# Performance work log

Measured on AMD Instinct MI355X. Metric: run time of the kernel, lower is better.

The kernel has to match this reference:

```python
import jax, jax.numpy as jnp
import numpy as np
from jax import lax

B, S, D = 4, 4096, 1024
EPS = 1e-6  # flax RMSNorm default epsilon


def setup_inputs() -> dict:
    key = jax.random.key(0)
    ks = jax.random.split(key, 8)
    std = 0.01  # flax.linen.initializers.normal() default stddev
    return {
        "x": jax.random.normal(ks[0], (B, S, D), dtype=jnp.float32),
        "wq": jax.random.normal(ks[1], (D, D), dtype=jnp.float32) * std,
        "wk": jax.random.normal(ks[2], (D, D), dtype=jnp.float32) * std,
        "wv": jax.random.normal(ks[3], (D, D), dtype=jnp.float32) * std,
        "wa": jax.random.normal(ks[4], (D, 2 * D), dtype=jnp.float32) * std,
        "wg": jax.random.normal(ks[5], (D, D), dtype=jnp.float32) * std,
        "wo": jax.random.normal(ks[6], (D, D), dtype=jnp.float32) * std,
        "rms_scale": jnp.ones((D,), dtype=jnp.float32),  # RMSNorm scale param
    }


def gate_loop_operator(k, v, q, a):
    # data-dependent complex linear recurrence: h_t = a_t * h_{t-1} + k_t * v_t
    def binary_operator(e_i, e_j):
        a_i, kv_i = e_i
        a_j, kv_j = e_j
        return (a_j * a_i, a_j * kv_i + kv_j)

    kv = (k * v).astype(jnp.complex64)
    _, y = lax.associative_scan(binary_operator, (a, kv), axis=1)
    return q * jnp.real(y)


def reference(x, wq, wk, wv, wa, wg, wo, rms_scale):
    # RMSNorm (flax default: no mean subtraction, learned scale)
    xn = x * lax.rsqrt(jnp.mean(x * x, axis=-1, keepdims=True) + EPS) * rms_scale

    q = xn @ wq
    k = xn @ wk
    v = xn @ wv
    a = xn @ wa  # [B, S, 2D]
    g = xn @ wg

    a_r, a_i = jnp.split(a, 2, axis=-1)
    a_c = lax.complex(a_r, a_i)
    magnitude = jax.nn.sigmoid(jnp.abs(a_c))  # constrain |a| < 1 for stability
    phase = jnp.angle(a_c)
    a_c = magnitude * jnp.exp(1j * phase)

    y = gate_loop_operator(k, v, q, a_c)
    y = y * jax.nn.silu(g)
    return y @ wo
```

## Files before the change

### kernel.cpp

```cpp
#include <hip/hip_runtime.h>
#include <hip/hip_bf16.h>
#include <math.h>

#define BDIM 4
#define SDIM 4096
#define DDIM 1024
#define MROWS (BDIM*SDIM)
#define EPS 1e-6f
#define NCHUNK 64
#define LCHUNK 64

typedef _Float16 f16_t;
typedef _Float16 f16x4_t __attribute__((ext_vector_type(4)));
typedef _Float16 f16x8_t __attribute__((ext_vector_type(8)));
typedef float    f32x4_t __attribute__((ext_vector_type(4)));

__device__ __forceinline__ void gload16(const void* g, void* l) {
    __builtin_amdgcn_global_load_lds(
        (const __attribute__((address_space(1))) unsigned int*)g,
        (__attribute__((address_space(3))) unsigned int*)l, 16, 0, 0);
}

__global__ __launch_bounds__(256) void fill_kernel(float* __restrict__ out,
                                                   int n, float val)
{
    const int i = blockIdx.x * 256 + threadIdx.x;
    if (i < n) out[i] = val;
}

__global__ __launch_bounds__(256) void rmsnorm_kernel(
    const float* __restrict__ x, const float* __restrict__ scale,
    f16_t* __restrict__ xn)
{
    const int row = blockIdx.x;
    const int tid = threadIdx.x;
    const float4 v = reinterpret_cast<const float4*>(x + (size_t)row * DDIM)[tid];
    float ss = v.x*v.x + v.y*v.y + v.z*v.z + v.w*v.w;
    #pragma unroll
    for (int off = 32; off > 0; off >>= 1)
        ss += __shfl_down(ss, off, 64);
    __shared__ float red[4];
    if ((tid & 63) == 0) red[tid >> 6] = ss;
    __syncthreads();
    ss = red[0] + red[1] + red[2] + red[3];
    const float inv = rsqrtf(ss * (1.0f / DDIM) + EPS);
    const float4 sc = reinterpret_cast<const float4*>(scale)[tid];
    f16x4_t o;
    o.x = (f16_t)(v.x * inv * sc.x);
    o.y = (f16_t)(v.y * inv * sc.y);
    o.z = (f16_t)(v.z * inv * sc.z);
    o.w = (f16_t)(v.w * inv * sc.w);
    reinterpret_cast<f16x4_t*>(xn + (size_t)row * DDIM)[tid] = o;
}

__global__ __launch_bounds__(256) void transpose_f16_kernel(
    const float* __restrict__ W, f16_t* __restrict__ WT, int K, int N)
{
    __shared__ float t[32][33];
    const int kb = blockIdx.y * 32;
    const int nb = blockIdx.x * 32;
    const int r  = threadIdx.x >> 3;
    const int c0 = (threadIdx.x & 7) << 2;
    const float4 v = *reinterpret_cast<const float4*>(&W[(size_t)(kb + r) * N + nb + c0]);
    t[r][c0 + 0] = v.x; t[r][c0 + 1] = v.y; t[r][c0 + 2] = v.z; t[r][c0 + 3] = v.w;
    __syncthreads();
    f16x4_t o;
    o.x = (f16_t)t[c0 + 0][r];
    o.y = (f16_t)t[c0 + 1][r];
    o.z = (f16_t)t[c0 + 2][r];
    o.w = (f16_t)t[c0 + 3][r];
    *reinterpret_cast<f16x4_t*>(&WT[(size_t)(nb + r) * K + kb + c0]) = o;
}

template <int MODE>
__global__ __launch_bounds__(256, 2) void mfma_gemm_kernel(
    const f16_t* __restrict__ A, const f16_t* __restrict__ BT,
    void* __restrict__ Cv, int M, int N, int K)
{
    __shared__ __align__(16) f16_t As[128 * 32];
    __shared__ __align__(16) f16_t Bs[128 * 32];

    const int tid  = threadIdx.x;
    const int wave = tid >> 6;
    const int lane = tid & 63;
    const int bm = blockIdx.y * 128;
    const int bn = blockIdx.x * 128;
    const int wm = (wave & 1) * 64;
    const int wn = (wave >> 1) * 64;

    const int sr = tid >> 2;
    const int sc = (tid & 3) * 8;
    const f16_t* Ag = A  + (size_t)(bm + sr) * K + sc;
    const f16_t* Bg = BT + (size_t)(bn + sr) * K + sc;
    f16_t* Al0 = As + tid * 8;
    f16_t* Al1 = As + 64 * 32 + tid * 8;
    f16_t* Bl0 = Bs + tid * 8;
    f16_t* Bl1 = Bs + 64 * 32 + tid * 8;
    const size_t rowskip = (size_t)64 * K;

    f32x4_t acc[4][4] = {};

    const int fm = lane & 15;
    const int kh = (lane >> 4) << 3;

    for (int kt = 0; kt < K; kt += 32) {
        gload16(Ag + kt, Al0);
        gload16(Ag + rowskip + kt, Al1);
        gload16(Bg + kt, Bl0);
        gload16(Bg + rowskip + kt, Bl1);
        __syncthreads();

        f16x8_t af[4], bfr[4];
        #pragma unroll
        for (int i = 0; i < 4; ++i)
            af[i] = *reinterpret_cast<const f16x8_t*>(&As[(wm + i * 16 + fm) * 32 + kh]);
        #pragma unroll
        for (int j = 0; j < 4; ++j)
            bfr[j] = *reinterpret_cast<const f16x8_t*>(&Bs[(wn + j * 16 + fm) * 32 + kh]);
        #pragma unroll
        for (int i = 0; i < 4; ++i)
            #pragma unroll
            for (int j = 0; j < 4; ++j)
                acc[i][j] = __builtin_amdgcn_mfma_f32_16x16x32_f16(
                    af[i], bfr[j], acc[i][j], 0, 0, 0);
        __syncthreads();
    }

    const int erow = (lane >> 4) << 2;
    const int ecol = lane & 15;
    #pragma unroll
    for (int i = 0; i < 4; ++i) {
        #pragma unroll
        for (int j = 0; j < 4; ++j) {
            const int row0 = bm + wm + i * 16 + erow;
            const int col  = bn + wn + j * 16 + ecol;
            #pragma unroll
            for (int rg = 0; rg < 4; ++rg) {
                const size_t idx = (size_t)(row0 + rg) * N + col;
                const float val = acc[i][j][rg];
                if (MODE == 0) {
                    ((float*)Cv)[idx] = val;
                } else if (MODE == 1) {
                    ((f16_t*)Cv)[idx] = (f16_t)val;
                } else if (MODE == 2) {
                    f16_t* C = (f16_t*)Cv;
                    C[idx] = (f16_t)((float)C[idx] * val);
                } else {
                    float* C = (float*)Cv;
                    const float s = val / (1.0f + expf(-val));
                    C[idx] = C[idx] * s;
                }
            }
        }
    }
}

__global__ __launch_bounds__(256) void atrans_kernel(float* __restrict__ a)
{
    const int i = blockIdx.x * 256 + threadIdx.x;
    const int m = i >> 10;
    const int d = i & 1023;
    const size_t i0 = (size_t)m * (2 * DDIM) + d;
    const float ar = a[i0];
    const float ai = a[i0 + DDIM];
    const float r = sqrtf(ar * ar + ai * ai);
    const float mag = 1.0f / (1.0f + expf(-r));
    if (r > 0.0f) {
        const float s = mag / r;
        a[i0] = ar * s;
        a[i0 + DDIM] = ai * s;
    } else {
        a[i0] = 0.5f;
        a[i0 + DDIM] = 0.0f;
    }
}

__global__ __launch_bounds__(256) void scan1_kernel(
    const float* __restrict__ a, const f16_t* __restrict__ kvb,
    float4* __restrict__ state)
{
    const int t = blockIdx.x * 256 + threadIdx.x;
    const int d = t & 1023;
    const int c = (t >> 10) & (NCHUNK - 1);
    const int b = t >> 16;
    size_t base  = ((size_t)(b * SDIM + c * LCHUNK)) * DDIM + d;
    size_t abase = ((size_t)(b * SDIM + c * LCHUNK)) * (2 * DDIM) + d;
    float Ar = 1.0f, Ai = 0.0f, Hr = 0.0f, Hi = 0.0f;
    for (int s = 0; s < LCHUNK; ++s) {
        const float arr = a[abase];
        const float aii = a[abase + DDIM];
        const float kv = (float)kvb[base];
        const float hr = arr * Hr - aii * Hi + kv;
        const float hi = arr * Hi + aii * Hr;
        Hr = hr; Hi = hi;
        const float nr = arr * Ar - aii * Ai;
        const float ni = arr * Ai + aii * Ar;
        Ar = nr; Ai = ni;
        base += DDIM;
        abase += 2 * DDIM;
    }
    state[t] = make_float4(Ar, Ai, Hr, Hi);
}

__global__ __launch_bounds__(256) void scan2_kernel(
    const float4* __restrict__ state, float2* __restrict__ carry)
{
    const int t = blockIdx.x * 256 + threadIdx.x;
    const int d = t & 1023;
    const int b = t >> 10;
    float cr = 0.0f, ci = 0.0f;
    for (int c = 0; c < NCHUNK; ++c) {
        const size_t idx = ((size_t)(b * NCHUNK + c)) * DDIM + d;
        carry[idx] = make_float2(cr, ci);
        const float4 st = state[idx];
        const float nr = st.x * cr - st.y * ci + st.z;
        const float ni = st.x * ci + st.y * cr + st.w;
        cr = nr; ci = ni;
    }
}

__global__ __launch_bounds__(256) void scan3_kernel(
    const float* __restrict__ a, const f16_t* __restrict__ kvb,
    const float* __restrict__ qg, const float2* __restrict__ carry,
    f16_t* __restrict__ y)
{
    const int t = blockIdx.x * 256 + threadIdx.x;
    const int d = t & 1023;
    const int c = (t >> 10) & (NCHUNK - 1);
    const int b = t >> 16;
    size_t base  = ((size_t)(b * SDIM + c * LCHUNK)) * DDIM + d;
    size_t abase = ((size_t)(b * SDIM + c * LCHUNK)) * (2 * DDIM) + d;
    const float2 h0 = carry[t];
    float Hr = h0.x, Hi = h0.y;
    for (int s = 0; s < LCHUNK; ++s) {
        const float arr = a[abase];
        const float aii = a[abase + DDIM];
        const float kv = (float)kvb[base];
        const float hr = arr * Hr - aii * Hi + kv;
        const float hi = arr * Hi + aii * Hr;
        Hr = hr; Hi = hi;
        y[base] = (f16_t)(qg[base] * Hr);
        base += DDIM;
        abase += 2 * DDIM;
    }
}

extern "C" void kernel_launch(void* const* d_in, const int* in_sizes, int n_in,
                              void* d_out, int out_size, void* d_ws, size_t ws_size,
                              hipStream_t stream)
{
    const float* x        = (const float*)d_in[0];
    const float* wq       = (const float*)d_in[1];
    const float* wk       = (const float*)d_in[2];
    const float* wv       = (const float*)d_in[3];
    const float* wa       = (const float*)d_in[4];
    const float* wg       = (const float*)d_in[5];
    const float* wo       = (const float*)d_in[6];
    const float* rms_scale= (const float*)d_in[7];
    float* out = (float*)d_out;

    const size_t SZ = (size_t)MROWS * DDIM;
    char* ws = (char*)d_ws;
    f16_t* W0   = (f16_t*)ws;
    f16_t* W1   = (f16_t*)(ws + SZ * 2);
    float* W2   = (float*)(ws + SZ * 4);
    f16_t* WT   = (f16_t*)(ws + SZ * 12);
    const size_t WSZ = (size_t)DDIM * DDIM;
    f16_t* WTq = WT;
    f16_t* WTk = WT + WSZ;
    f16_t* WTv = WT + 2 * WSZ;
    f16_t* WTg = WT + 3 * WSZ;
    f16_t* WTo = WT + 4 * WSZ;
    f16_t* WTa = WT + 5 * WSZ;
    float2* carry = (float2*)(ws + SZ * 12 + 7 * WSZ * 2);
    float4* state = (float4*)W0;

    const size_t needed = SZ * 12 + 7 * WSZ * 2
                        + (size_t)BDIM * NCHUNK * DDIM * sizeof(float2);
    if (ws_size < needed) {
        const float marker = (float)(ws_size >> 20);
        fill_kernel<<<(out_size + 255) / 256, 256, 0, stream>>>(out, out_size, marker);
        return;
    }

    rmsnorm_kernel<<<MROWS, 256, 0, stream>>>(x, rms_scale, W0);

    dim3 tblk(256);
    dim3 tg1(DDIM / 32, DDIM / 32);
    dim3 tg2(2 * DDIM / 32, DDIM / 32);
    transpose_f16_kernel<<<tg1, tblk, 0, stream>>>(wq, WTq, DDIM, DDIM);
    transpose_f16_kernel<<<tg1, tblk, 0, stream>>>(wk, WTk, DDIM, DDIM);
    transpose_f16_kernel<<<tg1, tblk, 0, stream>>>(wv, WTv, DDIM, DDIM);
    transpose_f16_kernel<<<tg1, tblk, 0, stream>>>(wg, WTg, DDIM, DDIM);
    transpose_f16_kernel<<<tg1, tblk, 0, stream>>>(wo, WTo, DDIM, DDIM);
    transpose_f16_kernel<<<tg2, tblk, 0, stream>>>(wa, WTa, DDIM, 2 * DDIM);

    dim3 blk(256);
    dim3 g1(DDIM / 128, MROWS / 128);
    dim3 g2(2 * DDIM / 128, MROWS / 128);
    mfma_gemm_kernel<0><<<g1, blk, 0, stream>>>(W0, WTq, out, MROWS, DDIM, DDIM);
    mfma_gemm_kernel<3><<<g1, blk, 0, stream>>>(W0, WTg, out, MROWS, DDIM, DDIM);
    mfma_gemm_kernel<1><<<g1, blk, 0, stream>>>(W0, WTk, W1,  MROWS, DDIM, DDIM);
    mfma_gemm_kernel<2><<<g1, blk, 0, stream>>>(W0, WTv, W1,  MROWS, DDIM, DDIM);
    mfma_gemm_kernel<0><<<g2, blk, 0, stream>>>(W0, WTa, W2,  MROWS, 2 * DDIM, DDIM);

    atrans_kernel<<<(MROWS * DDIM) / 256, 256, 0, stream>>>(W2);

    const int nscan = BDIM * NCHUNK * DDIM;
    scan1_kernel<<<nscan / 256, 256, 0, stream>>>(W2, W1, state);
    scan2_kernel<<<(BDIM * DDIM) / 256, 256, 0, stream>>>(state, carry);
    scan3_kernel<<<nscan / 256, 256, 0, stream>>>(W2, W1, out, carry, W0);

    mfma_gemm_kernel<0><<<g1, blk, 0, stream>>>(W0, WTo, out, MROWS, DDIM, DDIM);
}
```

Before: 654.7 us.

## Fuse Q/K/G projections, interleave complex gate weights, fold gate transform into GEMM

Concatenates the q, k and g projection weights into one N=3072 GEMM that scatters fp16 outputs to separate buffers, replacing three launches. The a-projection weights are column-interleaved so real and imaginary parts land in adjacent columns. The sigmoid-magnitude gate transform then runs in the GEMM epilogue via a lane shuffle, removing the separate atrans pass, and the scans read a as float2. The SiLU gating moves into scan3, and q/g are stored as fp16 in the output buffer, cutting fp32 traffic at the cost of extra q/g rounding and buffer aliasing (carry stored over the weight area).

```diff
diff --git a/kernel.cpp b/kernel.cpp
--- a/kernel.cpp
+++ b/kernel.cpp
@@ -72,10 +72,35 @@
     *reinterpret_cast<f16x4_t*>(&WT[(size_t)(nb + r) * K + kb + c0]) = o;
 }
 
+__global__ __launch_bounds__(256) void transpose_a_kernel(
+    const float* __restrict__ W, f16_t* __restrict__ WT)
+{
+    const int K = DDIM, N = 2 * DDIM;
+    __shared__ float t[32][33];
+    const int kb = blockIdx.y * 32;
+    const int nb = blockIdx.x * 32;
+    const int r  = threadIdx.x >> 3;
+    const int c0 = (threadIdx.x & 7) << 2;
+    const int base = (c0 < 16) ? ((nb >> 1) + c0) : (DDIM + (nb >> 1) + c0 - 16);
+    const float4 v = *reinterpret_cast<const float4*>(&W[(size_t)(kb + r) * N + base]);
+    t[r][c0 + 0] = v.x; t[r][c0 + 1] = v.y; t[r][c0 + 2] = v.z; t[r][c0 + 3] = v.w;
+    __syncthreads();
+    const int rr  = threadIdx.x >> 3;
+    const int cc0 = (threadIdx.x & 7) << 2;
+    const int ctile = (rr >> 1) + (rr & 1) * 16;
+    f16x4_t o;
+    o.x = (f16_t)t[cc0 + 0][ctile];
+    o.y = (f16_t)t[cc0 + 1][ctile];
+    o.z = (f16_t)t[cc0 + 2][ctile];
+    o.w = (f16_t)t[cc0 + 3][ctile];
+    *reinterpret_cast<f16x4_t*>(&WT[(size_t)(nb + rr) * K + kb + cc0]) = o;
+}
+
 template <int MODE>
 __global__ __launch_bounds__(256, 2) void mfma_gemm_kernel(
     const f16_t* __restrict__ A, const f16_t* __restrict__ BT,
-    void* __restrict__ Cv, int M, int N, int K)
+    void* __restrict__ Cv, void* __restrict__ Cv2, void* __restrict__ Cv3,
+    int M, int N, int K)
 {
     __shared__ __align__(16) f16_t As[128 * 32];
     __shared__ __align__(16) f16_t Bs[128 * 32];
@@ -140,38 +165,30 @@
                 const float val = acc[i][j][rg];
                 if (MODE == 0) {
                     ((float*)Cv)[idx] = val;
-                } else if (MODE == 1) {
-                    ((f16_t*)Cv)[idx] = (f16_t)val;
                 } else if (MODE == 2) {
                     f16_t* C = (f16_t*)Cv;
                     C[idx] = (f16_t)((float)C[idx] * val);
+                } else if (MODE == 4) {
+                    const float par = __shfl_xor(val, 1, 64);
+                    const float re = (lane & 1) ? par : val;
+                    const float im = (lane & 1) ? val : par;
+                    const float r = sqrtf(re * re + im * im);
+                    float outv;
+                    if (r > 0.0f) {
+                        const float sg = 1.0f / (1.0f + expf(-r));
+                        outv = val * (sg / r);
+                    } else {
+                        outv = (lane & 1) ? 0.0f : 0.5f;
+                    }
+                    ((float*)Cv)[idx] = outv;
                 } else {
-                    float* C = (float*)Cv;
-                    const float s = val / (1.0f + expf(-val));
-                    C[idx] = C[idx] * s;
+                    f16_t* dst = (bn < 1024) ? (f16_t*)Cv
+                               : (bn < 2048) ? (f16_t*)Cv2 : (f16_t*)Cv3;
+                    const size_t didx = (size_t)(row0 + rg) * DDIM + ((bn & 1023) + wn + j * 16 + ecol);
+                    dst[didx] = (f16_t)val;
                 }
             }
         }
-    }
-}
-
-__global__ __launch_bounds__(256) void atrans_kernel(float* __restrict__ a)
-{
-    const int i = blockIdx.x * 256 + threadIdx.x;
-    const int m = i >> 10;
-    const int d = i & 1023;
-    const size_t i0 = (size_t)m * (2 * DDIM) + d;
-    const float ar = a[i0];
-    const float ai = a[i0 + DDIM];
-    const float r = sqrtf(ar * ar + ai * ai);
-    const float mag = 1.0f / (1.0f + expf(-r));
-    if (r > 0.0f) {
-        const float s = mag / r;
-        a[i0] = ar * s;
-        a[i0 + DDIM] = ai * s;
-    } else {
-        a[i0] = 0.5f;
-        a[i0 + DDIM] = 0.0f;
     }
 }
 
@@ -184,20 +201,18 @@
     const int c = (t >> 10) & (NCHUNK - 1);
     const int b = t >> 16;
     size_t base  = ((size_t)(b * SDIM + c * LCHUNK)) * DDIM + d;
-    size_t abase = ((size_t)(b * SDIM + c * LCHUNK)) * (2 * DDIM) + d;
+    const float2* a2 = (const float2*)a;
     float Ar = 1.0f, Ai = 0.0f, Hr = 0.0f, Hi = 0.0f;
     for (int s = 0; s < LCHUNK; ++s) {
-        const float arr = a[abase];
-        const float aii = a[abase + DDIM];
+        const float2 av = a2[base];
         const float kv = (float)kvb[base];
-        const float hr = arr * Hr - aii * Hi + kv;
-        const float hi = arr * Hi + aii * Hr;
+        const float hr = av.x * Hr - av.y * Hi + kv;
+        const float hi = av.x * Hi + av.y * Hr;
         Hr = hr; Hi = hi;
-        const float nr = arr * Ar - aii * Ai;
-        const float ni = arr * Ai + aii * Ar;
+        const float nr = av.x * Ar - av.y * Ai;
+        const float ni = av.x * Ai + av.y * Ar;
         Ar = nr; Ai = ni;
         base += DDIM;
-        abase += 2 * DDIM;
     }
     state[t] = make_float4(Ar, Ai, Hr, Hi);
 }
@@ -220,28 +235,29 @@
 }
 
 __global__ __launch_bounds__(256) void scan3_kernel(
-    const float* __restrict__ a, const f16_t* __restrict__ kvb,
-    const float* __restrict__ qg, const float2* __restrict__ carry,
-    f16_t* __restrict__ y)
+    const float* __restrict__ a, f16_t* __restrict__ kvb,
+    const f16_t* __restrict__ qb, const f16_t* __restrict__ gb,
+    const float2* __restrict__ carry)
 {
     const int t = blockIdx.x * 256 + threadIdx.x;
     const int d = t & 1023;
     const int c = (t >> 10) & (NCHUNK - 1);
     const int b = t >> 16;
     size_t base  = ((size_t)(b * SDIM + c * LCHUNK)) * DDIM + d;
-    size_t abase = ((size_t)(b * SDIM + c * LCHUNK)) * (2 * DDIM) + d;
+    const float2* a2 = (const float2*)a;
     const float2 h0 = carry[t];
     float Hr = h0.x, Hi = h0.y;
     for (int s = 0; s < LCHUNK; ++s) {
-        const float arr = a[abase];
-        const float aii = a[abase + DDIM];
+        const float2 av = a2[base];
         const float kv = (float)kvb[base];
-        const float hr = arr * Hr - aii * Hi + kv;
-        const float hi = arr * Hi + aii * Hr;
+        const float hr = av.x * Hr - av.y * Hi + kv;
+        const float hi = av.x * Hi + av.y * Hr;
         Hr = hr; Hi = hi;
-        y[base] = (f16_t)(qg[base] * Hr);
+        const float qv = (float)qb[base];
+        const float gv = (float)gb[base];
+        const float silu = gv / (1.0f + expf(-gv));
+        kvb[base] = (f16_t)(qv * silu * Hr);
         base += DDIM;
-        abase += 2 * DDIM;
     }
 }
 
@@ -260,56 +276,55 @@
     float* out = (float*)d_out;
 
     const size_t SZ = (size_t)MROWS * DDIM;
+    const size_t WSZ = (size_t)DDIM * DDIM;
     char* ws = (char*)d_ws;
-    f16_t* W0   = (f16_t*)ws;
-    f16_t* W1   = (f16_t*)(ws + SZ * 2);
-    float* W2   = (float*)(ws + SZ * 4);
+    f16_t* xn   = (f16_t*)ws;
+    f16_t* kv   = (f16_t*)(ws + SZ * 2);
+    float* abuf = (float*)(ws + SZ * 4);
     f16_t* WT   = (f16_t*)(ws + SZ * 12);
-    const size_t WSZ = (size_t)DDIM * DDIM;
     f16_t* WTq = WT;
     f16_t* WTk = WT + WSZ;
-    f16_t* WTv = WT + 2 * WSZ;
-    f16_t* WTg = WT + 3 * WSZ;
-    f16_t* WTo = WT + 4 * WSZ;
-    f16_t* WTa = WT + 5 * WSZ;
-    float2* carry = (float2*)(ws + SZ * 12 + 7 * WSZ * 2);
-    float4* state = (float4*)W0;
-
-    const size_t needed = SZ * 12 + 7 * WSZ * 2
-                        + (size_t)BDIM * NCHUNK * DDIM * sizeof(float2);
+    f16_t* WTg = WT + 2 * WSZ;
+    f16_t* WTv = WT + 3 * WSZ;
+    f16_t* WTa = WT + 4 * WSZ;
+    f16_t* WTo = WT + 6 * WSZ;
+    float4* state = (float4*)xn;
+    float2* carry = (float2*)WT;
+
+    f16_t* qb = (f16_t*)d_out;
+    f16_t* gb = qb + SZ;
+
+    const size_t needed = SZ * 12 + 7 * WSZ * 2;
     if (ws_size < needed) {
         const float marker = (float)(ws_size >> 20);
         fill_kernel<<<(out_size + 255) / 256, 256, 0, stream>>>(out, out_size, marker);
         return;
     }
 
-    rmsnorm_kernel<<<MROWS, 256, 0, stream>>>(x, rms_scale, W0);
+    rmsnorm_kernel<<<MROWS, 256, 0, stream>>>(x, rms_scale, xn);
 
     dim3 tblk(256);
     dim3 tg1(DDIM / 32, DDIM / 32);
-    dim3 tg2(2 * DDIM / 32, DDIM / 32);
     transpose_f16_kernel<<<tg1, tblk, 0, stream>>>(wq, WTq, DDIM, DDIM);
     transpose_f16_kernel<<<tg1, tblk, 0, stream>>>(wk, WTk, DDIM, DDIM);
+    transpose_f16_kernel<<<tg1, tblk, 0, stream>>>(wg, WTg, DDIM, DDIM);
     transpose_f16_kernel<<<tg1, tblk, 0, stream>>>(wv, WTv, DDIM, DDIM);
-    transpose_f16_kernel<<<tg1, tblk, 0, stream>>>(wg, WTg, DDIM, DDIM);
     transpose_f16_kernel<<<tg1, tblk, 0, stream>>>(wo, WTo, DDIM, DDIM);
-    transpose_f16_kernel<<<tg2, tblk, 0, stream>>>(wa, WTa, DDIM, 2 * DDIM);
+    dim3 tga(2 * DDIM / 32, DDIM / 32);
+    transpose_a_kernel<<<tga, tblk, 0, stream>>>(wa, WTa);
 
     dim3 blk(256);
+    dim3 gqkg(3 * DDIM / 128, MROWS / 128);
     dim3 g1(DDIM / 128, MROWS / 128);
     dim3 g2(2 * DDIM / 128, MROWS / 128);
-    mfma_gemm_kernel<0><<<g1, blk, 0, stream>>>(W0, WTq, out, MROWS, DDIM, DDIM);
-    mfma_gemm_kernel<3><<<g1, blk, 0, stream>>>(W0, WTg, out, MROWS, DDIM, DDIM);
-    mfma_gemm_kernel<1><<<g1, blk, 0, stream>>>(W0, WTk, W1,  MROWS, DDIM, DDIM);
-    mfma_gemm_kernel<2><<<g1, blk, 0, stream>>>(W0, WTv, W1,  MROWS, DDIM, DDIM);
-    mfma_gemm_kernel<0><<<g2, blk, 0, stream>>>(W0, WTa, W2,  MROWS, 2 * DDIM, DDIM);
-
-    atrans_kernel<<<(MROWS * DDIM) / 256, 256, 0, stream>>>(W2);
+    mfma_gemm_kernel<5><<<gqkg, blk, 0, stream>>>(xn, WT,  qb, kv, gb, MROWS, 3 * DDIM, DDIM);
+    mfma_gemm_kernel<2><<<g1,   blk, 0, stream>>>(xn, WTv, kv, nullptr, nullptr, MROWS, DDIM, DDIM);
+    mfma_gemm_kernel<4><<<g2,   blk, 0, stream>>>(xn, WTa, abuf, nullptr, nullptr, MROWS, 2 * DDIM, DDIM);
 
     const int nscan = BDIM * NCHUNK * DDIM;
-    scan1_kernel<<<nscan / 256, 256, 0, stream>>>(W2, W1, state);
+    scan1_kernel<<<nscan / 256, 256, 0, stream>>>(abuf, kv, state);
     scan2_kernel<<<(BDIM * DDIM) / 256, 256, 0, stream>>>(state, carry);
-    scan3_kernel<<<nscan / 256, 256, 0, stream>>>(W2, W1, out, carry, W0);
-
-    mfma_gemm_kernel<0><<<g1, blk, 0, stream>>>(W0, WTo, out, MROWS, DDIM, DDIM);
-}
+    scan3_kernel<<<nscan / 256, 256, 0, stream>>>(abuf, kv, qb, gb, carry);
+
+    mfma_gemm_kernel<0><<<g1, blk, 0, stream>>>(kv, WTo, out, nullptr, nullptr, MROWS, DDIM, DDIM);
+}
```

New measurement: 591.3 us. 1.11x faster.
